# Performance work log

Measured on AMD Instinct MI355X. Metric: run time of the kernel, lower is better.

## Reference

```python
import jax, jax.numpy as jnp
import numpy as np

K = 1024          # num_embeddings
D = 64            # embedding_dim
COMMIT = 0.25     # commitment_cost
B, C, T = 16, 64, 2048


def setup_inputs() -> dict:
    key = jax.random.key(0)
    k1, k2 = jax.random.split(key)
    inputs = jax.random.normal(k1, (B, C, T), dtype=jnp.float32)
    # nn.Embedding weight initialized uniform(-1/K, 1/K)
    weight = jax.random.uniform(k2, (K, D), dtype=jnp.float32,
                                minval=-1.0 / K, maxval=1.0 / K)
    return {"inputs": inputs, "weight": weight}


def reference(inputs, weight):
    # inputs: [B, C, T] -> [B, T, C] with C == D
    x = jnp.transpose(inputs, (0, 2, 1))          # [B, T, D]
    flat = x.reshape(-1, D)                        # [N, D], N = B*T

    distances = (jnp.sum(flat ** 2, axis=1, keepdims=True)
                 + jnp.sum(weight ** 2, axis=1)
                 - 2.0 * jnp.matmul(flat, weight.T))
    encoding_indices = jnp.argmin(distances, axis=1)          # [N]

    encodings = jax.nn.one_hot(encoding_indices, K, dtype=jnp.float32)  # [N, K]
    quantized = weight[encoding_indices].reshape(x.shape)     # [B, T, D] (== matmul(encodings, weight))

    e_latent_loss = jnp.mean((jax.lax.stop_gradient(quantized) - x) ** 2)
    q_latent_loss = jnp.mean((quantized - jax.lax.stop_gradient(x)) ** 2)
    loss = q_latent_loss + COMMIT * e_latent_loss

    # straight-through estimator
    quantized_st = x + jax.lax.stop_gradient(quantized - x)

    avg_probs = jnp.mean(encodings, axis=0)                   # [K]
    perplexity = jnp.exp(-jnp.sum(avg_probs * jnp.log(avg_probs + 1e-10)))

    quant_out = jnp.transpose(quantized_st, (0, 2, 1))        # [B, C, T]
    return loss, quant_out, perplexity, encodings
```

## Files before the change

### kernel.cpp

```cpp
#include <hip/hip_runtime.h>
#include <cstdint>
#include <cstddef>

#define K_CODES 1024
#define D_DIM   64
#define T_SZ    2048
#define N_ROWS  32768
#define BCT     2097152

typedef const __attribute__((address_space(1))) uint32_t* gp1_t;
typedef __attribute__((address_space(3))) uint32_t*       lp3_t;
typedef __attribute__((ext_vector_type(8))) short         short8;
typedef __attribute__((ext_vector_type(4))) float         f32x4;
typedef __attribute__((ext_vector_type(4))) int           i32x4;


__device__ __forceinline__ ushort bf16_rne(float f) {
    uint32_t u = __builtin_bit_cast(uint32_t, f);
    u += 0x7FFFu + ((u >> 16) & 1u);
    return (ushort)(u >> 16);
}
__device__ __forceinline__ float bf16_f(ushort h) {
    uint32_t u = ((uint32_t)h) << 16;
    return __builtin_bit_cast(float, u);
}

__global__ __launch_bounds__(256) void k_prep(const float* __restrict__ w,
                                              float* __restrict__ esq,
                                              ushort* __restrict__ wpack,
                                              int* __restrict__ hist,
                                              double* __restrict__ loss_sum) {
    const int k = blockIdx.x * 256 + threadIdx.x;
    hist[k] = 0;
    if (k == 0) loss_sum[0] = 0.0;
    const int ct = k >> 4, cl = k & 15;
    double s = 0.0;
    for (int d = 0; d < 64; ++d) {
        const float x = w[k * 64 + d];
        s = fma((double)x, (double)x, s);
        const ushort hi = bf16_rne(x);
        const ushort lo = bf16_rne(x - bf16_f(hi));
        const int ks = d >> 5, g = (d >> 3) & 3, j = d & 7;
        const int lane = g * 16 + cl;
        const size_t base = ((size_t)(ct * 2 + ks)) * 2;
        wpack[((base + 0) * 64 + lane) * 8 + j] = hi;
        wpack[((base + 1) * 64 + lane) * 8 + j] = lo;
    }
    esq[k] = (float)s;
}

__global__ __launch_bounds__(512) void k_argmin(
        const float* __restrict__ in, const float* __restrict__ w,
        const float* __restrict__ esq, const ushort* __restrict__ wpack,
        int* __restrict__ hist, double* __restrict__ loss_sum,
        float* __restrict__ qout, float* __restrict__ enc) {
    __shared__ __align__(16) ushort lds_b[2][16384];
    __shared__ float  lds_esq[K_CODES];
    __shared__ int    smem_i1[128], smem_i2[128];
    __shared__ int    fin_s[128];
    __shared__ double redd[8];

    const int tid  = threadIdx.x;
    const int lane = tid & 63;
    const int wv   = tid >> 6;
    const int cl   = lane & 15;
    const int g    = lane >> 4;
    const int n0   = blockIdx.x * 128;
    const int b    = n0 >> 11;
    const int t0   = n0 & (T_SZ - 1);

    lds_esq[tid]       = esq[tid];
    lds_esq[tid + 512] = esq[tid + 512];

    const int t_row = t0 + wv * 16 + cl;
    short8 ah[2], al[2];
#pragma unroll
    for (int ks = 0; ks < 2; ++ks) {
        short8 h, l;
#pragma unroll
        for (int j = 0; j < 8; ++j) {
            const int d = ks * 32 + g * 8 + j;
            const float x = in[(size_t)b * 131072 + (size_t)d * T_SZ + t_row];
            const ushort hb = bf16_rne(x);
            h[j] = (short)hb;
            l[j] = (short)bf16_rne(x - bf16_f(hb));
        }
        ah[ks] = h;
        al[ks] = l;
    }

#define STAGEW(BUF, CH)                                                        \
    {                                                                          \
        _Pragma("unroll")                                                      \
        for (int r = 0; r < 4; ++r) {                                          \
            const int li = r * 512 + tid;                                      \
            const ushort* gsrc = wpack + (size_t)(CH)*16384 + (size_t)li * 8;  \
            ushort* ldst = &lds_b[BUF][li * 8];                                \
            __builtin_amdgcn_global_load_lds((gp1_t)gsrc, (lp3_t)ldst, 16, 0, 0);\
        }                                                                      \
    }

    STAGEW(0, 0)
    __syncthreads();

    f32x4 m1v = {-1e30f, -1e30f, -1e30f, -1e30f};
    f32x4 m2v = {-1e30f, -1e30f, -1e30f, -1e30f};
    i32x4 i1v = {0, 0, 0, 0};
    i32x4 i2v = {0, 0, 0, 0};

    int buf = 0;
    for (int ch = 0; ch < 8; ++ch) {
        if (ch < 7) STAGEW(buf ^ 1, ch + 1)
#pragma unroll
        for (int ctl = 0; ctl < 8; ++ctl) {
            const int ct = ch * 8 + ctl;
            const int c  = ct * 16 + cl;
            const float e2 = -0.5f * lds_esq[c];
            f32x4 accP = {e2, e2, e2, e2};
            f32x4 accQ = {0.f, 0.f, 0.f, 0.f};
#pragma unroll
            for (int ks = 0; ks < 2; ++ks) {
                const short8 bh = *(const short8*)&lds_b[buf][(((ctl * 2 + ks) * 2 + 0) * 64 + lane) * 8];
                const short8 bl = *(const short8*)&lds_b[buf][(((ctl * 2 + ks) * 2 + 1) * 64 + lane) * 8];
                accP = __builtin_amdgcn_mfma_f32_16x16x32_bf16(ah[ks], bh, accP, 0, 0, 0);
                accQ = __builtin_amdgcn_mfma_f32_16x16x32_bf16(ah[ks], bl, accQ, 0, 0, 0);
                accQ = __builtin_amdgcn_mfma_f32_16x16x32_bf16(al[ks], bh, accQ, 0, 0, 0);
            }
#pragma unroll
            for (int reg = 0; reg < 4; ++reg) {
                const float v = accP[reg] + accQ[reg];
                const bool gt1 = v > m1v[reg];
                const bool gt2 = v > m2v[reg];
                const float nm2 = gt1 ? m1v[reg] : (gt2 ? v : m2v[reg]);
                const int   ni2 = gt1 ? i1v[reg] : (gt2 ? c : i2v[reg]);
                m1v[reg] = gt1 ? v : m1v[reg];
                i1v[reg] = gt1 ? c : i1v[reg];
                m2v[reg] = nm2;
                i2v[reg] = ni2;
            }
        }
        __syncthreads();
        buf ^= 1;
    }

#pragma unroll
    for (int off = 1; off < 16; off <<= 1) {
#pragma unroll
        for (int reg = 0; reg < 4; ++reg) {
            const float pm1 = __shfl_xor(m1v[reg], off);
            const int   pi1 = __shfl_xor(i1v[reg], off);
            const float pm2 = __shfl_xor(m2v[reg], off);
            const int   pi2 = __shfl_xor(i2v[reg], off);
            const bool ours = (m1v[reg] > pm1) ||
                              (m1v[reg] == pm1 && i1v[reg] < pi1);
            float nm1, nm2; int ni1, ni2;
            if (ours) {
                nm1 = m1v[reg]; ni1 = i1v[reg];
                const bool pb = (pm1 > m2v[reg]) ||
                                (pm1 == m2v[reg] && pi1 < i2v[reg]);
                nm2 = pb ? pm1 : m2v[reg];
                ni2 = pb ? pi1 : i2v[reg];
            } else {
                nm1 = pm1; ni1 = pi1;
                const bool ob = (m1v[reg] > pm2) ||
                                (m1v[reg] == pm2 && i1v[reg] < pi2);
                nm2 = ob ? m1v[reg] : pm2;
                ni2 = ob ? i1v[reg] : pi2;
            }
            m1v[reg] = nm1; i1v[reg] = ni1;
            m2v[reg] = nm2; i2v[reg] = ni2;
        }
    }
    if (cl == 0) {
#pragma unroll
        for (int reg = 0; reg < 4; ++reg) {
            smem_i1[wv * 16 + g * 4 + reg] = i1v[reg];
            smem_i2[wv * 16 + g * 4 + reg] = i2v[reg];
        }
    }
    __syncthreads();

    if (lane < 16) {
        const int rloc = wv * 16 + lane;
        const int ii1 = smem_i1[rloc], ii2 = smem_i2[rloc];
        const int t = t0 + rloc;
        double v1 = 0.0, v2 = 0.0;
        for (int d = 0; d < 64; ++d) {
            const double x = (double)in[(size_t)b * 131072 + (size_t)d * T_SZ + t];
            const double a = (double)w[ii1 * 64 + d] - x;
            const double cdd = (double)w[ii2 * 64 + d] - x;
            v1 = fma(a, a, v1);
            v2 = fma(cdd, cdd, v2);
        }
        int fin;
        if (v1 < v2)      fin = ii1;
        else if (v2 < v1) fin = ii2;
        else              fin = (ii1 < ii2) ? ii1 : ii2;
        fin_s[rloc] = fin;
        atomicAdd(&hist[fin], 1);
    }
    __syncthreads();

    double sq = 0.0;
#pragma unroll
    for (int it = 0; it < 16; ++it) {
        const int idx = it * 512 + tid;
        const int d  = idx >> 7;
        const int tt = idx & 127;
        const float q = w[fin_s[tt] * 64 + d];
        const size_t go = (size_t)b * 131072 + (size_t)d * T_SZ + t0 + tt;
        const float x = in[go];
        qout[go] = q;
        const double dd = (double)q - (double)x;
        sq = fma(dd, dd, sq);
    }
    for (int off = 32; off > 0; off >>= 1) sq += __shfl_down(sq, off);
    if (lane == 0) redd[wv] = sq;

#pragma unroll 1
    for (int rr = 0; rr < 16; ++rr) {
        const int rloc = wv * 16 + rr;
        const int f = fin_s[rloc];
        float* ebase = enc + (((size_t)(n0 + rloc)) << 10);
#pragma unroll
        for (int jj = 0; jj < 8; ++jj) {
            const int col = jj * 128 + lane * 2;
            float2 v;
            v.x = (col == f)     ? 1.0f : 0.0f;
            v.y = (col + 1 == f) ? 1.0f : 0.0f;
            *(float2*)(ebase + col) = v;
        }
    }

    __syncthreads();
    if (tid == 0) {
        double s = 0.0;
#pragma unroll
        for (int i = 0; i < 8; ++i) s += redd[i];
        atomicAdd(loss_sum, s);
    }
}

__global__ __launch_bounds__(256) void k_final(const int* __restrict__ hist,
                                               const double* __restrict__ loss_sum,
                                               float* __restrict__ out_loss,
                                               float* __restrict__ out_perp) {
    __shared__ double red[256];
    const int tid = threadIdx.x;
    double h = 0.0;
    for (int k = tid; k < K_CODES; k += 256) {
        const double p = (double)hist[k] / (double)N_ROWS;
        h += p * log(p + 1e-10);
    }
    red[tid] = h;
    __syncthreads();
#pragma unroll
    for (int st = 128; st > 0; st >>= 1) {
        if (tid < st) red[tid] += red[tid + st];
        __syncthreads();
    }
    if (tid == 0) {
        out_perp[0] = (float)exp(-red[0]);
        const double mean = loss_sum[0] / (double)BCT;
        out_loss[0] = (float)(1.25 * mean);
    }
}

extern "C" void kernel_launch(void* const* d_in, const int* in_sizes, int n_in,
                              void* d_out, int out_size, void* d_ws, size_t ws_size,
                              hipStream_t stream) {
    const float* in = (const float*)d_in[0];
    const float* w  = (const float*)d_in[1];

    float* out      = (float*)d_out;
    float* out_loss = out;
    float* out_q    = out + 1;
    float* out_perp = out + 1 + BCT;
    float* out_enc  = out + 2 + BCT;

    char*   ws       = (char*)d_ws;
    int*    ws_hist  = (int*)ws;
    double* ws_loss  = (double*)(ws + 4096);
    float*  ws_esq   = (float*)(ws + 8192);
    ushort* ws_wpack = (ushort*)(ws + 16384);

    k_prep  <<<4,   256, 0, stream>>>(w, ws_esq, ws_wpack, ws_hist, ws_loss);
    k_argmin<<<256, 512, 0, stream>>>(in, w, ws_esq, ws_wpack, ws_hist,
                                      ws_loss, out_q, out_enc);
    k_final <<<1,   256, 0, stream>>>(ws_hist, ws_loss, out_loss, out_perp);
}
```

Before: 207.8 us.

## Halve argmin block size, parallelize prep and rescoring, stage codewords in LDS

The argmin kernel now processes 64 rows per block with 256 threads across 512 blocks, with launch bounds asking for two blocks per CU, so more blocks are resident and more CUs are used. The prep kernel splits each codeword's 64 dimensions over 8 threads and sums with shuffles. The fp64 rescoring of the top-2 candidates is spread over 4 lanes per row instead of one. The selected codewords are first gathered into padded LDS so the transposed quantized-output write reads conflict-free LDS instead of scattered global memory. In exchange, each block fetches the full codebook for only half as many rows, doubling total codebook traffic.

```diff
diff --git a/kernel.cpp b/kernel.cpp
--- a/kernel.cpp
+++ b/kernel.cpp
@@ -30,12 +30,15 @@
                                               ushort* __restrict__ wpack,
                                               int* __restrict__ hist,
                                               double* __restrict__ loss_sum) {
-    const int k = blockIdx.x * 256 + threadIdx.x;
-    hist[k] = 0;
-    if (k == 0) loss_sum[0] = 0.0;
+    const int gtid = blockIdx.x * 256 + threadIdx.x;
+    const int k = gtid >> 3, grp = gtid & 7;
+    if (gtid < K_CODES) hist[gtid] = 0;
+    if (gtid == 0) loss_sum[0] = 0.0;
     const int ct = k >> 4, cl = k & 15;
     double s = 0.0;
-    for (int d = 0; d < 64; ++d) {
+#pragma unroll
+    for (int jj = 0; jj < 8; ++jj) {
+        const int d = grp * 8 + jj;
         const float x = w[k * 64 + d];
         s = fma((double)x, (double)x, s);
         const ushort hi = bf16_rne(x);
@@ -46,31 +49,32 @@
         wpack[((base + 0) * 64 + lane) * 8 + j] = hi;
         wpack[((base + 1) * 64 + lane) * 8 + j] = lo;
     }
-    esq[k] = (float)s;
-}
-
-__global__ __launch_bounds__(512) void k_argmin(
+    s += __shfl_xor(s, 1); s += __shfl_xor(s, 2); s += __shfl_xor(s, 4);
+    if (grp == 0) esq[k] = (float)s;
+}
+
+__global__ __launch_bounds__(256, 2) void k_argmin(
         const float* __restrict__ in, const float* __restrict__ w,
         const float* __restrict__ esq, const ushort* __restrict__ wpack,
         int* __restrict__ hist, double* __restrict__ loss_sum,
         float* __restrict__ qout, float* __restrict__ enc) {
     __shared__ __align__(16) ushort lds_b[2][16384];
     __shared__ float  lds_esq[K_CODES];
-    __shared__ int    smem_i1[128], smem_i2[128];
-    __shared__ int    fin_s[128];
-    __shared__ double redd[8];
+    __shared__ int    smem_i1[64], smem_i2[64];
+    __shared__ int    fin_s[64];
+    __shared__ double redd[4];
 
     const int tid  = threadIdx.x;
     const int lane = tid & 63;
     const int wv   = tid >> 6;
     const int cl   = lane & 15;
     const int g    = lane >> 4;
-    const int n0   = blockIdx.x * 128;
+    const int n0   = blockIdx.x * 64;
     const int b    = n0 >> 11;
     const int t0   = n0 & (T_SZ - 1);
 
-    lds_esq[tid]       = esq[tid];
-    lds_esq[tid + 512] = esq[tid + 512];
+#pragma unroll
+    for (int r = 0; r < 4; ++r) lds_esq[r * 256 + tid] = esq[r * 256 + tid];
 
     const int t_row = t0 + wv * 16 + cl;
     short8 ah[2], al[2];
@@ -92,8 +96,8 @@
 #define STAGEW(BUF, CH)                                                        \
     {                                                                          \
         _Pragma("unroll")                                                      \
-        for (int r = 0; r < 4; ++r) {                                          \
-            const int li = r * 512 + tid;                                      \
+        for (int r = 0; r < 8; ++r) {                                          \
+            const int li = r * 256 + tid;                                      \
             const ushort* gsrc = wpack + (size_t)(CH)*16384 + (size_t)li * 8;  \
             ushort* ldst = &lds_b[BUF][li * 8];                                \
             __builtin_amdgcn_global_load_lds((gp1_t)gsrc, (lp3_t)ldst, 16, 0, 0);\
@@ -180,36 +184,51 @@
     }
     __syncthreads();
 
-    if (lane < 16) {
-        const int rloc = wv * 16 + lane;
+    {
+        const int rloc = wv * 16 + (lane >> 2);
+        const int quar = lane & 3;
         const int ii1 = smem_i1[rloc], ii2 = smem_i2[rloc];
         const int t = t0 + rloc;
         double v1 = 0.0, v2 = 0.0;
-        for (int d = 0; d < 64; ++d) {
+#pragma unroll
+        for (int j = 0; j < 16; ++j) {
+            const int d = quar * 16 + j;
             const double x = (double)in[(size_t)b * 131072 + (size_t)d * T_SZ + t];
-            const double a = (double)w[ii1 * 64 + d] - x;
-            const double cdd = (double)w[ii2 * 64 + d] - x;
+            const double a  = (double)w[ii1 * 64 + d] - x;
+            const double cc = (double)w[ii2 * 64 + d] - x;
             v1 = fma(a, a, v1);
-            v2 = fma(cdd, cdd, v2);
-        }
-        int fin;
-        if (v1 < v2)      fin = ii1;
-        else if (v2 < v1) fin = ii2;
-        else              fin = (ii1 < ii2) ? ii1 : ii2;
-        fin_s[rloc] = fin;
-        atomicAdd(&hist[fin], 1);
+            v2 = fma(cc, cc, v2);
+        }
+        v1 += __shfl_xor(v1, 1); v1 += __shfl_xor(v1, 2);
+        v2 += __shfl_xor(v2, 1); v2 += __shfl_xor(v2, 2);
+        if (quar == 0) {
+            int fin;
+            if (v1 < v2)      fin = ii1;
+            else if (v2 < v1) fin = ii2;
+            else              fin = (ii1 < ii2) ? ii1 : ii2;
+            fin_s[rloc] = fin;
+            atomicAdd(&hist[fin], 1);
+        }
+    }
+    __syncthreads();
+
+    float* lds_q = (float*)&lds_b[0][0];
+#pragma unroll
+    for (int r = 0; r < 16; ++r) {
+        const int idx = r * 256 + tid;
+        const int row = idx >> 6, d = idx & 63;
+        lds_q[row * 65 + d] = w[fin_s[row] * 64 + d];
     }
     __syncthreads();
 
     double sq = 0.0;
 #pragma unroll
     for (int it = 0; it < 16; ++it) {
-        const int idx = it * 512 + tid;
-        const int d  = idx >> 7;
-        const int tt = idx & 127;
-        const float q = w[fin_s[tt] * 64 + d];
+        const int idx = it * 256 + tid;
+        const int tt = idx & 63, d = idx >> 6;
         const size_t go = (size_t)b * 131072 + (size_t)d * T_SZ + t0 + tt;
         const float x = in[go];
+        const float q = lds_q[tt * 65 + d];
         qout[go] = q;
         const double dd = (double)q - (double)x;
         sq = fma(dd, dd, sq);
@@ -234,9 +253,7 @@
 
     __syncthreads();
     if (tid == 0) {
-        double s = 0.0;
-#pragma unroll
-        for (int i = 0; i < 8; ++i) s += redd[i];
+        double s = redd[0] + redd[1] + redd[2] + redd[3];
         atomicAdd(loss_sum, s);
     }
 }
@@ -284,8 +301,8 @@
     float*  ws_esq   = (float*)(ws + 8192);
     ushort* ws_wpack = (ushort*)(ws + 16384);
 
-    k_prep  <<<4,   256, 0, stream>>>(w, ws_esq, ws_wpack, ws_hist, ws_loss);
-    k_argmin<<<256, 512, 0, stream>>>(in, w, ws_esq, ws_wpack, ws_hist,
+    k_prep  <<<32,  256, 0, stream>>>(w, ws_esq, ws_wpack, ws_hist, ws_loss);
+    k_argmin<<<512, 256, 0, stream>>>(in, w, ws_esq, ws_wpack, ws_hist,
                                       ws_loss, out_q, out_enc);
     k_final <<<1,   256, 0, stream>>>(ws_hist, ws_loss, out_loss, out_perp);
 }
```

After: 188.7 us. 9.2% less time.
